# Optimization experiments

Hardware: AMD Instinct MI355X
Metric: run time of the kernel (lower is better)

The kernel has to match this reference:

```python
import jax, jax.numpy as jnp
import numpy as np
from jax import lax

NPOINT, RADIUS, NSAMPLE, EPS = 2048, 0.1, 32, 1e-5


def setup_inputs() -> dict:
    key = jax.random.key(0)
    ks = jax.random.split(key, 8)
    B, N, D, CIN, COUT, DEPTH = 4, 8192, 29, 32, 64, 2
    return {
        "xyz": jax.random.uniform(ks[0], (B, 3, N), jnp.float32),
        "points": jax.random.normal(ks[1], (B, D, N), jnp.float32),
        "proj_w": jax.random.normal(ks[2], (COUT, CIN), jnp.float32) * 0.05,
        "proj_g": jnp.ones((COUT,), jnp.float32),
        "proj_b": jnp.zeros((COUT,), jnp.float32),
        "w1": jax.random.normal(ks[3], (DEPTH, COUT, COUT), jnp.float32) * 0.05,
        "g1": jnp.ones((DEPTH, COUT), jnp.float32),
        "b1": jnp.zeros((DEPTH, COUT), jnp.float32),
        "w2": jax.random.normal(ks[4], (DEPTH, COUT, COUT), jnp.float32) * 0.05,
        "g2": jnp.ones((DEPTH, COUT), jnp.float32),
        "b2": jnp.zeros((DEPTH, COUT), jnp.float32),
    }


def fps(xyz, npoint):
    # xyz: [B,N,3] -> idx [B,npoint]; deterministic start at index 0
    B, N, _ = xyz.shape
    def body(carry, _):
        dist, far = carry  # [B,N], [B]
        centroid = jnp.take_along_axis(xyz, far[:, None, None], axis=1)  # [B,1,3]
        d = jnp.sum((xyz - centroid) ** 2, -1)
        dist = jnp.minimum(dist, d)
        return (dist, jnp.argmax(dist, -1).astype(jnp.int32)), far
    init = (jnp.full((B, N), 1e10, xyz.dtype), jnp.zeros((B,), jnp.int32))
    _, idx = lax.scan(body, init, None, length=npoint)
    return jnp.transpose(idx)  # [B,npoint]


def ball_query(radius, nsample, xyz, new_xyz):
    # matches torch query_ball_point: invalid -> N, sort, take first nsample, backfill
    N = xyz.shape[1]
    sqr = (jnp.sum(new_xyz ** 2, -1)[:, :, None]
           + jnp.sum(xyz ** 2, -1)[:, None, :]
           - 2.0 * jnp.einsum("bsc,bnc->bsn", new_xyz, xyz))  # [B,S,N]
    cand = jnp.where(sqr <= radius * radius, jnp.arange(N, dtype=jnp.int32), jnp.int32(N))
    neg, _ = lax.top_k(-cand, nsample)
    idx = -neg  # nsample smallest indices, ascending
    first = idx[:, :, :1]
    return jnp.where(idx == N, first, idx)  # [B,S,K]


def gather_nb(p, idx):
    # p [B,N,C], idx [B,S,K] -> [B,S,K,C]
    return jax.vmap(lambda pb, ib: pb[ib])(p, idx)


def _conv(x, w):
    # 1x1 conv: w [O,C], x [B,C,K,S]
    return jnp.einsum("oc,bcks->boks", w, x)


def _bn(x, g, b):
    # training-mode BatchNorm2d over (B,K,S) per channel
    m = jnp.mean(x, (0, 2, 3), keepdims=True)
    v = jnp.var(x, (0, 2, 3), keepdims=True)
    return g[None, :, None, None] * (x - m) * lax.rsqrt(v + EPS) + b[None, :, None, None]


def reference(xyz, points, proj_w, proj_g, proj_b, w1, g1, b1, w2, g2, b2):
    xyz_t = jnp.transpose(xyz, (0, 2, 1))      # [B,N,3]
    pts_t = jnp.transpose(points, (0, 2, 1))   # [B,N,D]
    fidx = fps(xyz_t, NPOINT)                  # [B,S]
    new_xyz = jnp.take_along_axis(xyz_t, fidx[:, :, None], axis=1)  # [B,S,3]
    idx = ball_query(RADIUS, NSAMPLE, xyz_t, new_xyz)               # [B,S,K]
    grouped_xyz = gather_nb(xyz_t, idx) - new_xyz[:, :, None, :]    # [B,S,K,3]
    grouped_pts = gather_nb(pts_t, idx)                             # [B,S,K,D]
    new_points = jnp.concatenate([grouped_xyz, grouped_pts], -1)    # [B,S,K,3+D]
    x = jnp.transpose(new_points, (0, 3, 2, 1))                     # [B,C,K,S]
    x = jax.nn.relu(_bn(_conv(x, proj_w), proj_g, proj_b))
    for d in range(w1.shape[0]):
        idn = x
        x = jax.nn.relu(_bn(_conv(x, w1[d]), g1[d], b1[d]))
        x = _bn(_conv(x, w2[d]), g2[d], b2[d])
        x = jax.nn.relu(x + idn)
    feat = jnp.max(x, axis=2)                  # [B,Cout,S]
    return jnp.transpose(new_xyz, (0, 2, 1)), feat
```

## Files before the change

### kernel.cpp

```cpp
#include <hip/hip_runtime.h>
#include <cstdint>
#include <cstddef>

#define NPTS    8192
#define NPT     2048
#define KNB     32
#define NB      4
#define DPTS    29
#define CINP    32
#define CO      64
#define KS      (KNB*NPT)
#define TELEM   ((size_t)NB*CO*KS)
#define MCNT    262144.0f
#define BNEPS   1e-5f
#define FTHR    1024
#define FWAVES  (FTHR/64)
#define FPT     8

#define FPS_STEP(J)                                                      \
    {                                                                    \
        float dx = __fsub_rn(px##J, cx);                                 \
        float dy = __fsub_rn(py##J, cy);                                 \
        float dz = __fsub_rn(pz##J, cz);                                 \
        float dd = __fadd_rn(__fadd_rn(__fmul_rn(dx, dx),                \
                                       __fmul_rn(dy, dy)),               \
                             __fmul_rn(dz, dz));                         \
        float nd = fminf(d##J, dd);                                      \
        d##J = nd;                                                       \
        bool gt = nd > tb;                                               \
        tb = gt ? nd : tb;                                               \
        jj = gt ? J : jj;                                                \
    }

static __device__ __forceinline__ unsigned long long umax64(unsigned long long a,
                                                            unsigned long long b) {
    return a > b ? a : b;
}

__global__ __launch_bounds__(FTHR, 1)
void fps_kernel(const float* __restrict__ xyz,
                float* __restrict__ out0) {
    const int b = blockIdx.x;
    const int t = threadIdx.x;
    const int lane = t & 63;
    const int wid  = t >> 6;
    const float* xb = xyz + (size_t)b * 3 * NPTS;
    const int base = t * FPT;

    extern __shared__ float smem[];
    float* sx = smem;
    float* sy = sx + NPTS;
    float* sz = sy + NPTS;
    unsigned long long* skey = (unsigned long long*)(sz + NPTS);

    float px0,px1,px2,px3,px4,px5,px6,px7;
    float py0,py1,py2,py3,py4,py5,py6,py7;
    float pz0,pz1,pz2,pz3,pz4,pz5,pz6,pz7;
    float d0,d1,d2,d3,d4,d5,d6,d7;
    {
        const float4* x4 = (const float4*)(xb + base);
        const float4* y4 = (const float4*)(xb + NPTS + base);
        const float4* z4 = (const float4*)(xb + 2 * NPTS + base);
        float4* lx4 = (float4*)(sx + base);
        float4* ly4 = (float4*)(sy + base);
        float4* lz4 = (float4*)(sz + base);
        float4 v;
        v = x4[0]; lx4[0] = v; px0 =v.x; px1 =v.y; px2 =v.z; px3 =v.w;
        v = x4[1]; lx4[1] = v; px4 =v.x; px5 =v.y; px6 =v.z; px7 =v.w;
        v = y4[0]; ly4[0] = v; py0 =v.x; py1 =v.y; py2 =v.z; py3 =v.w;
        v = y4[1]; ly4[1] = v; py4 =v.x; py5 =v.y; py6 =v.z; py7 =v.w;
        v = z4[0]; lz4[0] = v; pz0 =v.x; pz1 =v.y; pz2 =v.z; pz3 =v.w;
        v = z4[1]; lz4[1] = v; pz4 =v.x; pz5 =v.y; pz6 =v.z; pz7 =v.w;
        d0=d1=d2=d3=d4=d5=d6=d7 = 1e10f;
    }

    float cx = xb[0], cy = xb[NPTS], cz = xb[2 * NPTS];
    float* ob = out0 + (size_t)b * 3 * NPT;
    if (t == 0) { ob[0] = cx; ob[NPT] = cy; ob[2 * NPT] = cz; }

    for (int i = 1; i < NPT; ++i) {
        float tb = -1.0f;
        int   jj = 0;
        FPS_STEP(0) FPS_STEP(1) FPS_STEP(2) FPS_STEP(3)
        FPS_STEP(4) FPS_STEP(5) FPS_STEP(6) FPS_STEP(7)
        const int gidx = base + jj;

        float wm = tb;
#pragma unroll
        for (int o = 32; o > 0; o >>= 1) wm = fmaxf(wm, __shfl_xor(wm, o, 64));
        unsigned long long eq = __ballot(tb == wm);
        const int lwin = __ffsll((long long)eq) - 1;
        const int wgid = __shfl(gidx, lwin, 64);

        const int par = i & 1;
        if (lane == 0)
            skey[par * FWAVES + wid] =
                (((unsigned long long)__float_as_uint(wm)) << 32) |
                (unsigned int)(~(unsigned int)wgid);
        __syncthreads();

        const ulonglong2* sk2 = (const ulonglong2*)(skey + par * FWAVES);
        ulonglong2 k0 = sk2[0], k1 = sk2[1], k2 = sk2[2], k3 = sk2[3];
        ulonglong2 k4 = sk2[4], k5 = sk2[5], k6 = sk2[6], k7 = sk2[7];
        unsigned long long m0 = umax64(k0.x, k0.y);
        unsigned long long m1 = umax64(k1.x, k1.y);
        unsigned long long m2 = umax64(k2.x, k2.y);
        unsigned long long m3 = umax64(k3.x, k3.y);
        unsigned long long m4 = umax64(k4.x, k4.y);
        unsigned long long m5 = umax64(k5.x, k5.y);
        unsigned long long m6 = umax64(k6.x, k6.y);
        unsigned long long m7 = umax64(k7.x, k7.y);
        unsigned long long kbest = umax64(umax64(umax64(m0, m1), umax64(m2, m3)),
                                          umax64(umax64(m4, m5), umax64(m6, m7)));
        const int widx = (int)(~(unsigned int)kbest);

        cx = sx[widx]; cy = sy[widx]; cz = sz[widx];
        if (t == 0) { ob[i] = cx; ob[NPT + i] = cy; ob[2 * NPT + i] = cz; }
    }
}

__global__ __launch_bounds__(256) void ballq_kernel(const float* __restrict__ xyz,
                                                    const float* __restrict__ out0,
                                                    int* __restrict__ idx) {
    const int gw   = (blockIdx.x * 256 + threadIdx.x) >> 6;
    const int lane = threadIdx.x & 63;
    const int b  = gw >> 11;
    const int si = gw & 2047;
    const float* xb = xyz + (size_t)b * 3 * NPTS;

    const float cx = out0[b * 3 * NPT + si];
    const float cy = out0[b * 3 * NPT + NPT + si];
    const float cz = out0[b * 3 * NPT + 2*NPT + si];
    const float csum = __fadd_rn(__fadd_rn(__fmul_rn(cx, cx), __fmul_rn(cy, cy)),
                                 __fmul_rn(cz, cz));
    const float R2 = (float)(0.1 * 0.1);

    __shared__ int buf[4][KNB];
    int* mybuf = buf[threadIdx.x >> 6];

    int cnt = 0;
    for (int n0 = 0; n0 < NPTS && cnt < KNB; n0 += 64) {
        const int i = n0 + lane;
        float pxv = xb[i], pyv = xb[NPTS + i], pzv = xb[2 * NPTS + i];
        float ps = __fadd_rn(__fadd_rn(__fmul_rn(pxv, pxv), __fmul_rn(pyv, pyv)),
                             __fmul_rn(pzv, pzv));
        float dot = __fmaf_rn(pzv, cz, __fmaf_rn(pyv, cy, __fmul_rn(pxv, cx)));
        float sqr = __fsub_rn(__fadd_rn(csum, ps), __fadd_rn(dot, dot));
        bool hit = (sqr <= R2);
        unsigned long long m = __ballot(hit);
        int pos = cnt + __popcll(m & ((1ull << lane) - 1ull));
        if (hit && pos < KNB) mybuf[pos] = i;
        cnt += __popcll(m);
    }
    __syncthreads();
    int c = cnt < KNB ? cnt : KNB;
    int first = (cnt > 0) ? mybuf[0] : 0;
    if (lane < KNB) {
        int v = (lane < c) ? mybuf[lane] : first;
        idx[((size_t)gw << 5) + lane] = v;
    }
}

__global__ __launch_bounds__(256) void proj_kernel(const float* __restrict__ xyz,
                                                   const float* __restrict__ points,
                                                   const float* __restrict__ out0,
                                                   const int* __restrict__ idx,
                                                   const float* __restrict__ W,
                                                   float* __restrict__ out,
                                                   float* __restrict__ stats) {
    const int p = blockIdx.x * 256 + threadIdx.x;
    const int b = p >> 16;
    const int q = p & 65535;
    const int k = q >> 11;
    const int s = q & 2047;
    const int tid = threadIdx.x;

    __shared__ float ssum[CO], ssq[CO];
    if (tid < CO) { ssum[tid] = 0.f; ssq[tid] = 0.f; }
    __syncthreads();

    const int j = idx[((size_t)(b * NPT + s) << 5) + k];
    const float* xb = xyz + (size_t)b * 3 * NPTS;
    float a[CINP];
    a[0] = xb[j]            - out0[b * 3 * NPT + s];
    a[1] = xb[NPTS + j]     - out0[b * 3 * NPT + NPT + s];
    a[2] = xb[2*NPTS + j]   - out0[b * 3 * NPT + 2*NPT + s];
    const float* pb = points + (size_t)b * DPTS * NPTS;
#pragma unroll
    for (int c = 0; c < DPTS; ++c) a[3 + c] = pb[c * NPTS + j];

    const size_t obase = (size_t)b * CO * KS + q;
    for (int o = 0; o < CO; ++o) {
        float acc = 0.f;
#pragma unroll
        for (int c = 0; c < CINP; ++c) acc = __fmaf_rn(W[o * CINP + c], a[c], acc);
        out[obase + (size_t)o * KS] = acc;
        float s1 = acc, s2 = acc * acc;
#pragma unroll
        for (int off = 32; off > 0; off >>= 1) {
            s1 += __shfl_xor(s1, off, 64);
            s2 += __shfl_xor(s2, off, 64);
        }
        if ((tid & 63) == 0) { atomicAdd(&ssum[o], s1); atomicAdd(&ssq[o], s2); }
    }
    __syncthreads();
    if (tid < CO) {
        atomicAdd(&stats[tid], ssum[tid]);
        atomicAdd(&stats[CO + tid], ssq[tid]);
    }
}

template <bool HAS_IDN, bool WRITE_ACT>
__global__ __launch_bounds__(256) void conv_bn_kernel(const float* in,
                                                      const float* idn,
                                                      const float* __restrict__ stats_in,
                                                      const float* __restrict__ gamma,
                                                      const float* __restrict__ beta,
                                                      const float* __restrict__ W,
                                                      float* act_out,
                                                      float* out,
                                                      float* __restrict__ stats_out) {
    const int p = blockIdx.x * 256 + threadIdx.x;
    const int b = p >> 16;
    const int q = p & 65535;
    const int tid = threadIdx.x;

    __shared__ float ssc[CO], ssh[CO], ssum[CO], ssq[CO];
    if (tid < CO) {
        const float Minv = 1.0f / MCNT;
        float m = stats_in[tid] * Minv;
        float v = stats_in[CO + tid] * Minv - m * m;
        float scl = gamma[tid] * rsqrtf(v + BNEPS);
        ssc[tid] = scl;
        ssh[tid] = beta[tid] - m * scl;
        ssum[tid] = 0.f; ssq[tid] = 0.f;
    }
    __syncthreads();

    const size_t base = (size_t)b * CO * KS + q;
    float a[CO];
#pragma unroll
    for (int c = 0; c < CO; ++c) {
        float v = __fmaf_rn(ssc[c], in[base + (size_t)c * KS], ssh[c]);
        if (HAS_IDN) v += idn[base + (size_t)c * KS];
        v = fmaxf(v, 0.0f);
        a[c] = v;
        if (WRITE_ACT) act_out[base + (size_t)c * KS] = v;
    }
    for (int o = 0; o < CO; ++o) {
        float acc = 0.f;
#pragma unroll
        for (int c = 0; c < CO; ++c) acc = __fmaf_rn(W[o * CO + c], a[c], acc);
        out[base + (size_t)o * KS] = acc;
        float s1 = acc, s2 = acc * acc;
#pragma unroll
        for (int off = 32; off > 0; off >>= 1) {
            s1 += __shfl_xor(s1, off, 64);
            s2 += __shfl_xor(s2, off, 64);
        }
        if ((tid & 63) == 0) { atomicAdd(&ssum[o], s1); atomicAdd(&ssq[o], s2); }
    }
    __syncthreads();
    if (tid < CO) {
        atomicAdd(&stats_out[tid], ssum[tid]);
        atomicAdd(&stats_out[CO + tid], ssq[tid]);
    }
}

__global__ __launch_bounds__(256) void final_kernel(const float* __restrict__ y2,
                                                    const float* __restrict__ idn,
                                                    const float* __restrict__ stats,
                                                    const float* __restrict__ gamma,
                                                    const float* __restrict__ beta,
                                                    float* __restrict__ feat) {
    const int p = blockIdx.x * 256 + threadIdx.x;
    const int s = p & 2047;
    const int o = (p >> 11) & 63;
    const int b = p >> 17;
    const float Minv = 1.0f / MCNT;
    float m = stats[o] * Minv;
    float v = stats[CO + o] * Minv - m * m;
    float scl = gamma[o] * rsqrtf(v + BNEPS);
    float sh  = beta[o] - m * scl;
    const size_t base = (size_t)b * CO * KS + (size_t)o * KS + s;
    float mx = -1e30f;
#pragma unroll
    for (int k = 0; k < KNB; ++k) {
        float val = __fmaf_rn(scl, y2[base + (size_t)k * NPT], sh) + idn[base + (size_t)k * NPT];
        val = fmaxf(val, 0.0f);
        mx = fmaxf(mx, val);
    }
    feat[p] = mx;
}

__global__ void zero_kernel(float* p, int n) {
    int i = blockIdx.x * blockDim.x + threadIdx.x;
    if (i < n) p[i] = 0.f;
}

extern "C" void kernel_launch(void* const* d_in, const int* in_sizes, int n_in,
                              void* d_out, int out_size, void* d_ws, size_t ws_size,
                              hipStream_t stream) {
    (void)in_sizes; (void)n_in; (void)out_size; (void)ws_size;
    const float* xyz    = (const float*)d_in[0];
    const float* points = (const float*)d_in[1];
    const float* proj_w = (const float*)d_in[2];
    const float* proj_g = (const float*)d_in[3];
    const float* proj_b = (const float*)d_in[4];
    const float* w1     = (const float*)d_in[5];
    const float* g1     = (const float*)d_in[6];
    const float* b1     = (const float*)d_in[7];
    const float* w2     = (const float*)d_in[8];
    const float* g2     = (const float*)d_in[9];
    const float* b2     = (const float*)d_in[10];

    float* out0 = (float*)d_out;
    float* feat = (float*)d_out + NB * 3 * NPT;

    float* stats = (float*)d_ws;
    int*   idx   = (int*)((float*)d_ws + 1024);
    float* A     = (float*)(idx + NB * NPT * KNB);
    float* B     = A + TELEM;

    const size_t fps_lds = (size_t)(3 * NPTS) * sizeof(float)
                         + 2 * FWAVES * sizeof(unsigned long long);

    hipLaunchKernelGGL(zero_kernel, dim3(3), dim3(256), 0, stream, stats, 5 * 2 * CO);
    hipLaunchKernelGGL(fps_kernel, dim3(NB), dim3(FTHR), fps_lds, stream, xyz, out0);
    hipLaunchKernelGGL(ballq_kernel, dim3(2048), dim3(256), 0, stream, xyz, out0, idx);
    hipLaunchKernelGGL(proj_kernel, dim3(1024), dim3(256), 0, stream,
                       xyz, points, out0, idx, proj_w, A, stats);
    hipLaunchKernelGGL((conv_bn_kernel<false, true>), dim3(1024), dim3(256), 0, stream,
                       A, (const float*)nullptr, stats, proj_g, proj_b, w1,
                       B, A, stats + 128);
    hipLaunchKernelGGL((conv_bn_kernel<false, false>), dim3(1024), dim3(256), 0, stream,
                       A, (const float*)nullptr, stats + 128, g1, b1, w2,
                       (float*)nullptr, A, stats + 256);
    hipLaunchKernelGGL((conv_bn_kernel<true, true>), dim3(1024), dim3(256), 0, stream,
                       A, B, stats + 256, g2, b2, w1 + CO * CO,
                       B, A, stats + 384);
    hipLaunchKernelGGL((conv_bn_kernel<false, false>), dim3(1024), dim3(256), 0, stream,
                       A, (const float*)nullptr, stats + 384, g1 + CO, b1 + CO, w2 + CO * CO,
                       (float*)nullptr, A, stats + 512);
    hipLaunchKernelGGL(final_kernel, dim3(2048), dim3(256), 0, stream,
                       A, B, stats + 512, g2 + CO, b2 + CO, feat);
}
```

Before: 2.925 ms.

## Spatially bin FPS points per wave and skip waves beyond current max distance

The FPS kernel now sorts the points of each batch into a 4x4x4 spatial grid so that each wave owns a compact cluster of points, and computes a per-wave bounding box. At each iteration a wave skips its distance update when the box's distance to the new centroid cannot lower the wave's current maximum, and reuses its cached key. It also replaces shuffle reductions with DPP reductions, resolves ties by smallest global index, and buffers the sampled coordinates in LDS, writing them out once at the end. The counting sort adds setup work and LDS atomics, and the skip only pays off if whole waves are frequently pruned.

```diff
diff --git a/kernel.cpp b/kernel.cpp
--- a/kernel.cpp
+++ b/kernel.cpp
@@ -25,16 +25,66 @@
         float dd = __fadd_rn(__fadd_rn(__fmul_rn(dx, dx),                \
                                        __fmul_rn(dy, dy)),               \
                              __fmul_rn(dz, dz));                         \
-        float nd = fminf(d##J, dd);                                      \
-        d##J = nd;                                                       \
-        bool gt = nd > tb;                                               \
-        tb = gt ? nd : tb;                                               \
-        jj = gt ? J : jj;                                                \
+        d##J = fminf(d##J, dd);                                          \
+    }
+
+#define CELL_OF(X, Y, Z, OUT)                                            \
+    {                                                                    \
+        int ix = (int)((X) * 4.0f); ix = ix < 0 ? 0 : (ix > 3 ? 3 : ix); \
+        int iy = (int)((Y) * 4.0f); iy = iy < 0 ? 0 : (iy > 3 ? 3 : iy); \
+        int iz = (int)((Z) * 4.0f); iz = iz < 0 ? 0 : (iz > 3 ? 3 : iz); \
+        OUT = (ix & 1) | ((iy & 1) << 1) | ((iz & 1) << 2) |             \
+              ((ix & 2) << 2) | ((iy & 2) << 3) | ((iz & 2) << 4);       \
     }
 
 static __device__ __forceinline__ unsigned long long umax64(unsigned long long a,
                                                             unsigned long long b) {
     return a > b ? a : b;
+}
+
+static __device__ __forceinline__ float dppmax_f32_to63(float v) {
+    int x = __float_as_int(v), y;
+    y = __builtin_amdgcn_update_dpp(0, x, 0x111, 0xf, 0xf, true);
+    x = __float_as_int(fmaxf(__int_as_float(x), __int_as_float(y)));
+    y = __builtin_amdgcn_update_dpp(0, x, 0x112, 0xf, 0xf, true);
+    x = __float_as_int(fmaxf(__int_as_float(x), __int_as_float(y)));
+    y = __builtin_amdgcn_update_dpp(0, x, 0x114, 0xf, 0xf, true);
+    x = __float_as_int(fmaxf(__int_as_float(x), __int_as_float(y)));
+    y = __builtin_amdgcn_update_dpp(0, x, 0x118, 0xf, 0xf, true);
+    x = __float_as_int(fmaxf(__int_as_float(x), __int_as_float(y)));
+    y = __builtin_amdgcn_update_dpp(0, x, 0x142, 0xa, 0xf, true);
+    x = __float_as_int(fmaxf(__int_as_float(x), __int_as_float(y)));
+    y = __builtin_amdgcn_update_dpp(0, x, 0x143, 0xc, 0xf, true);
+    x = __float_as_int(fmaxf(__int_as_float(x), __int_as_float(y)));
+    return __int_as_float(x);
+}
+
+static __device__ __forceinline__ float dppmin_f32_to63(float v) {
+    int x = __float_as_int(v), y;
+    y = __builtin_amdgcn_update_dpp(x, x, 0x111, 0xf, 0xf, false);
+    x = __float_as_int(fminf(__int_as_float(x), __int_as_float(y)));
+    y = __builtin_amdgcn_update_dpp(x, x, 0x112, 0xf, 0xf, false);
+    x = __float_as_int(fminf(__int_as_float(x), __int_as_float(y)));
+    y = __builtin_amdgcn_update_dpp(x, x, 0x114, 0xf, 0xf, false);
+    x = __float_as_int(fminf(__int_as_float(x), __int_as_float(y)));
+    y = __builtin_amdgcn_update_dpp(x, x, 0x118, 0xf, 0xf, false);
+    x = __float_as_int(fminf(__int_as_float(x), __int_as_float(y)));
+    y = __builtin_amdgcn_update_dpp(x, x, 0x142, 0xa, 0xf, false);
+    x = __float_as_int(fminf(__int_as_float(x), __int_as_float(y)));
+    y = __builtin_amdgcn_update_dpp(x, x, 0x143, 0xc, 0xf, false);
+    x = __float_as_int(fminf(__int_as_float(x), __int_as_float(y)));
+    return __int_as_float(x);
+}
+
+static __device__ __forceinline__ int dppmin_i32_to63(int v) {
+    int x = v, y;
+    y = __builtin_amdgcn_update_dpp(x, x, 0x111, 0xf, 0xf, false); x = y < x ? y : x;
+    y = __builtin_amdgcn_update_dpp(x, x, 0x112, 0xf, 0xf, false); x = y < x ? y : x;
+    y = __builtin_amdgcn_update_dpp(x, x, 0x114, 0xf, 0xf, false); x = y < x ? y : x;
+    y = __builtin_amdgcn_update_dpp(x, x, 0x118, 0xf, 0xf, false); x = y < x ? y : x;
+    y = __builtin_amdgcn_update_dpp(x, x, 0x142, 0xa, 0xf, false); x = y < x ? y : x;
+    y = __builtin_amdgcn_update_dpp(x, x, 0x143, 0xc, 0xf, false); x = y < x ? y : x;
+    return x;
 }
 
 __global__ __launch_bounds__(FTHR, 1)
@@ -51,12 +101,14 @@
     float* sx = smem;
     float* sy = sx + NPTS;
     float* sz = sy + NPTS;
-    unsigned long long* skey = (unsigned long long*)(sz + NPTS);
-
-    float px0,px1,px2,px3,px4,px5,px6,px7;
-    float py0,py1,py2,py3,py4,py5,py6,py7;
-    float pz0,pz1,pz2,pz3,pz4,pz5,pz6,pz7;
-    float d0,d1,d2,d3,d4,d5,d6,d7;
+    int*   region = (int*)(sz + NPTS);
+    int*   sgid = region;
+    float* so   = (float*)region;
+    unsigned long long* skey = (unsigned long long*)((float*)region + 3 * NPT);
+    int* scnt = region + NPTS;
+    int* soff = scnt + 64;
+
+    float4 vx0, vx1, vy0, vy1, vz0, vz1;
     {
         const float4* x4 = (const float4*)(xb + base);
         const float4* y4 = (const float4*)(xb + NPTS + base);
@@ -64,39 +116,99 @@
         float4* lx4 = (float4*)(sx + base);
         float4* ly4 = (float4*)(sy + base);
         float4* lz4 = (float4*)(sz + base);
-        float4 v;
-        v = x4[0]; lx4[0] = v; px0 =v.x; px1 =v.y; px2 =v.z; px3 =v.w;
-        v = x4[1]; lx4[1] = v; px4 =v.x; px5 =v.y; px6 =v.z; px7 =v.w;
-        v = y4[0]; ly4[0] = v; py0 =v.x; py1 =v.y; py2 =v.z; py3 =v.w;
-        v = y4[1]; ly4[1] = v; py4 =v.x; py5 =v.y; py6 =v.z; py7 =v.w;
-        v = z4[0]; lz4[0] = v; pz0 =v.x; pz1 =v.y; pz2 =v.z; pz3 =v.w;
-        v = z4[1]; lz4[1] = v; pz4 =v.x; pz5 =v.y; pz6 =v.z; pz7 =v.w;
-        d0=d1=d2=d3=d4=d5=d6=d7 = 1e10f;
-    }
+        vx0 = x4[0]; lx4[0] = vx0;  vx1 = x4[1]; lx4[1] = vx1;
+        vy0 = y4[0]; ly4[0] = vy0;  vy1 = y4[1]; ly4[1] = vy1;
+        vz0 = z4[0]; lz4[0] = vz0;  vz1 = z4[1]; lz4[1] = vz1;
+    }
+    if (t < 64) scnt[t] = 0;
+    __syncthreads();
+
+#define P_CNT(PX, PY, PZ) { int cc; CELL_OF(PX, PY, PZ, cc); atomicAdd(&scnt[cc], 1); }
+    P_CNT(vx0.x, vy0.x, vz0.x) P_CNT(vx0.y, vy0.y, vz0.y)
+    P_CNT(vx0.z, vy0.z, vz0.z) P_CNT(vx0.w, vy0.w, vz0.w)
+    P_CNT(vx1.x, vy1.x, vz1.x) P_CNT(vx1.y, vy1.y, vz1.y)
+    P_CNT(vx1.z, vy1.z, vz1.z) P_CNT(vx1.w, vy1.w, vz1.w)
+    __syncthreads();
+    if (t == 0) {
+        int off = 0;
+        for (int c2 = 0; c2 < 64; ++c2) { int n = scnt[c2]; soff[c2] = off; off += n; }
+    }
+    __syncthreads();
+#define P_SCAT(PX, PY, PZ, GI)                                           \
+    { int cc; CELL_OF(PX, PY, PZ, cc);                                   \
+      int pos = atomicAdd(&soff[cc], 1);                                 \
+      sgid[((pos & 7) << 10) + (pos >> 3)] = (GI); }
+    P_SCAT(vx0.x, vy0.x, vz0.x, base + 0) P_SCAT(vx0.y, vy0.y, vz0.y, base + 1)
+    P_SCAT(vx0.z, vy0.z, vz0.z, base + 2) P_SCAT(vx0.w, vy0.w, vz0.w, base + 3)
+    P_SCAT(vx1.x, vy1.x, vz1.x, base + 4) P_SCAT(vx1.y, vy1.y, vz1.y, base + 5)
+    P_SCAT(vx1.z, vy1.z, vz1.z, base + 6) P_SCAT(vx1.w, vy1.w, vz1.w, base + 7)
+    __syncthreads();
+
+    int g0 = sgid[0*1024 + t], g1 = sgid[1*1024 + t],
+        g2 = sgid[2*1024 + t], g3 = sgid[3*1024 + t],
+        g4 = sgid[4*1024 + t], g5 = sgid[5*1024 + t],
+        g6 = sgid[6*1024 + t], g7 = sgid[7*1024 + t];
+    float px0 = sx[g0], py0 = sy[g0], pz0 = sz[g0];
+    float px1 = sx[g1], py1 = sy[g1], pz1 = sz[g1];
+    float px2 = sx[g2], py2 = sy[g2], pz2 = sz[g2];
+    float px3 = sx[g3], py3 = sy[g3], pz3 = sz[g3];
+    float px4 = sx[g4], py4 = sy[g4], pz4 = sz[g4];
+    float px5 = sx[g5], py5 = sy[g5], pz5 = sz[g5];
+    float px6 = sx[g6], py6 = sy[g6], pz6 = sz[g6];
+    float px7 = sx[g7], py7 = sy[g7], pz7 = sz[g7];
+    float d0, d1, d2, d3, d4, d5, d6, d7;
+    d0 = d1 = d2 = d3 = d4 = d5 = d6 = d7 = 1e10f;
+
+    float mnx = fminf(fminf(fminf(px0,px1),fminf(px2,px3)),fminf(fminf(px4,px5),fminf(px6,px7)));
+    float mxx = fmaxf(fmaxf(fmaxf(px0,px1),fmaxf(px2,px3)),fmaxf(fmaxf(px4,px5),fmaxf(px6,px7)));
+    float mny = fminf(fminf(fminf(py0,py1),fminf(py2,py3)),fminf(fminf(py4,py5),fminf(py6,py7)));
+    float mxy = fmaxf(fmaxf(fmaxf(py0,py1),fmaxf(py2,py3)),fmaxf(fmaxf(py4,py5),fmaxf(py6,py7)));
+    float mnz = fminf(fminf(fminf(pz0,pz1),fminf(pz2,pz3)),fminf(fminf(pz4,pz5),fminf(pz6,pz7)));
+    float mxz = fmaxf(fmaxf(fmaxf(pz0,pz1),fmaxf(pz2,pz3)),fmaxf(fmaxf(pz4,pz5),fmaxf(pz6,pz7)));
+    const float bminx = __int_as_float(__builtin_amdgcn_readlane(__float_as_int(dppmin_f32_to63(mnx)), 63));
+    const float bmaxx = __int_as_float(__builtin_amdgcn_readlane(__float_as_int(dppmax_f32_to63(mxx)), 63));
+    const float bminy = __int_as_float(__builtin_amdgcn_readlane(__float_as_int(dppmin_f32_to63(mny)), 63));
+    const float bmaxy = __int_as_float(__builtin_amdgcn_readlane(__float_as_int(dppmax_f32_to63(mxy)), 63));
+    const float bminz = __int_as_float(__builtin_amdgcn_readlane(__float_as_int(dppmin_f32_to63(mnz)), 63));
+    const float bmaxz = __int_as_float(__builtin_amdgcn_readlane(__float_as_int(dppmax_f32_to63(mxz)), 63));
+
+    __syncthreads();
 
     float cx = xb[0], cy = xb[NPTS], cz = xb[2 * NPTS];
-    float* ob = out0 + (size_t)b * 3 * NPT;
-    if (t == 0) { ob[0] = cx; ob[NPT] = cy; ob[2 * NPT] = cz; }
+    if (t == 0) { so[0] = cx; so[NPT] = cy; so[2 * NPT] = cz; }
+
+    float wmax = 3.0e38f;
+    unsigned long long kpack = 0;
 
     for (int i = 1; i < NPT; ++i) {
-        float tb = -1.0f;
-        int   jj = 0;
-        FPS_STEP(0) FPS_STEP(1) FPS_STEP(2) FPS_STEP(3)
-        FPS_STEP(4) FPS_STEP(5) FPS_STEP(6) FPS_STEP(7)
-        const int gidx = base + jj;
-
-        float wm = tb;
-#pragma unroll
-        for (int o = 32; o > 0; o >>= 1) wm = fmaxf(wm, __shfl_xor(wm, o, 64));
-        unsigned long long eq = __ballot(tb == wm);
-        const int lwin = __ffsll((long long)eq) - 1;
-        const int wgid = __shfl(gidx, lwin, 64);
-
+        float ddx = fmaxf(fmaxf(bminx - cx, cx - bmaxx), 0.0f);
+        float ddy = fmaxf(fmaxf(bminy - cy, cy - bmaxy), 0.0f);
+        float ddz = fmaxf(fmaxf(bminz - cz, cz - bmaxz), 0.0f);
+        float bd2 = ddx * ddx + ddy * ddy + ddz * ddz;
+        if (!(bd2 * 0.9999f >= wmax)) {
+            FPS_STEP(0) FPS_STEP(1) FPS_STEP(2) FPS_STEP(3)
+            FPS_STEP(4) FPS_STEP(5) FPS_STEP(6) FPS_STEP(7)
+            float tb = fmaxf(fmaxf(fmaxf(d0,d1),fmaxf(d2,d3)),
+                             fmaxf(fmaxf(d4,d5),fmaxf(d6,d7)));
+            int bg = 0x7fffffff;
+            if (d0 == tb) bg = g0 < bg ? g0 : bg;
+            if (d1 == tb) bg = g1 < bg ? g1 : bg;
+            if (d2 == tb) bg = g2 < bg ? g2 : bg;
+            if (d3 == tb) bg = g3 < bg ? g3 : bg;
+            if (d4 == tb) bg = g4 < bg ? g4 : bg;
+            if (d5 == tb) bg = g5 < bg ? g5 : bg;
+            if (d6 == tb) bg = g6 < bg ? g6 : bg;
+            if (d7 == tb) bg = g7 < bg ? g7 : bg;
+            float wm_s = __int_as_float(
+                __builtin_amdgcn_readlane(__float_as_int(dppmax_f32_to63(tb)), 63));
+            int cand = (tb == wm_s) ? bg : 0x7fffffff;
+            int wgid = __builtin_amdgcn_readlane(dppmin_i32_to63(cand), 63);
+            wmax = wm_s;
+            kpack = (((unsigned long long)__float_as_uint(wm_s)) << 32) |
+                    (unsigned)(~(unsigned)wgid);
+        }
         const int par = i & 1;
-        if (lane == 0)
-            skey[par * FWAVES + wid] =
-                (((unsigned long long)__float_as_uint(wm)) << 32) |
-                (unsigned int)(~(unsigned int)wgid);
+        if (lane == 63) skey[par * FWAVES + wid] = kpack;
         __syncthreads();
 
         const ulonglong2* sk2 = (const ulonglong2*)(skey + par * FWAVES);
@@ -115,8 +227,12 @@
         const int widx = (int)(~(unsigned int)kbest);
 
         cx = sx[widx]; cy = sy[widx]; cz = sz[widx];
-        if (t == 0) { ob[i] = cx; ob[NPT + i] = cy; ob[2 * NPT + i] = cz; }
-    }
+        if (t == 0) { so[i] = cx; so[NPT + i] = cy; so[2 * NPT + i] = cz; }
+    }
+
+    __syncthreads();
+    float* ob = out0 + (size_t)b * 3 * NPT;
+    for (int r = t; r < 3 * NPT; r += FTHR) ob[r] = so[r];
 }
 
 __global__ __launch_bounds__(256) void ballq_kernel(const float* __restrict__ xyz,
@@ -323,7 +439,8 @@
     float* B     = A + TELEM;
 
     const size_t fps_lds = (size_t)(3 * NPTS) * sizeof(float)
-                         + 2 * FWAVES * sizeof(unsigned long long);
+                         + (size_t)NPTS * sizeof(int)
+                         + 128 * sizeof(int);
 
     hipLaunchKernelGGL(zero_kernel, dim3(3), dim3(256), 0, stream, stats, 5 * 2 * CO);
     hipLaunchKernelGGL(fps_kernel, dim3(NB), dim3(FTHR), fps_lds, stream, xyz, out0);
```

Measured after the change: 3.195 ms. 1.09x slower.
